# Kernel optimization log

Measured on AMD Instinct MI355X. Metric: run time of the kernel, lower is better.

The kernel has to match this reference:

```python
import jax, jax.numpy as jnp
import numpy as np

# SigKernel config (from init_kwargs)
SCALES = np.array([1.0], dtype=np.float32)
S0, S1 = 0.0, 1.0   # s0, S
T0, T1 = 0.0, 1.0   # t0, T
REFINEMENT = 1.0    # refinement_factor (new grid == old grid => interp is identity)


def _interpolate(X, t_min, t_max, refinement_factor):
    """Linear interpolation of batched paths (B, L, D) onto a refined uniform grid."""
    L = X.shape[1]
    new_L = int(refinement_factor * (L - 1)) + 1
    t = jnp.linspace(t_min, t_max, L)
    t_new = jnp.linspace(t_min, t_max, new_L)
    interp_ch = lambda ch: jnp.interp(t_new, t, ch)            # (L,) -> (new_L,)
    interp_path = lambda p: jax.vmap(interp_ch, in_axes=1, out_axes=1)(p)
    return jax.vmap(interp_path)(X)


def _solve_pde_single(inc):
    """Second-order finite-difference Goursat solve of K_st = inc * K.

    inc: (m, m) increment matrix. Returns K[m, m] (scalar), with boundary K[i,0]=K[0,j]=1.
    Wavefront recursion over the 2m-1 interior antidiagonals via lax.scan; each
    diagonal is stored as a length-(m+1) vector indexed by the row i (col j = d - i).
    """
    m = inc.shape[0]
    n = m + 1
    idx = jnp.arange(n)
    K0 = jnp.where(idx == 0, 1.0, 0.0)   # antidiagonal d=0
    K1 = jnp.where(idx <= 1, 1.0, 0.0)   # antidiagonal d=1

    def step(carry, d):
        Km2, Km1 = carry                 # diagonals d-2, d-1
        j = d - idx
        ir = jnp.clip(idx - 1, 0, m - 1)
        jc = jnp.clip(j - 1, 0, m - 1)
        a = inc[ir, jc]                  # inc[i-1, j-1] along the diagonal
        f1 = 1.0 + 0.5 * a + (a * a) * (1.0 / 12.0)
        f2 = 1.0 - (a * a) * (1.0 / 12.0)
        # K[i,j] = (K[i,j-1] + K[i-1,j]) * f1 - K[i-1,j-1] * f2
        Kij = (Km1 + jnp.roll(Km1, 1)) * f1 - jnp.roll(Km2, 1) * f2
        Kd = jnp.where((idx == 0) | (j == 0), 1.0, Kij)      # boundary = 1
        Kd = jnp.where((j >= 0) & (j <= m), Kd, 0.0)         # off-diagonal mask
        return (Km1, Kd), None

    (_, Klast), _ = jax.lax.scan(step, (K0, K1), jnp.arange(2, 2 * m + 1))
    return Klast[m]  # K at (m, m)


def _sig_kernel_matrix(X, Y, scale):
    # linear static kernel k(x,y) = scale^2 <x,y>  =>  grid increments of k
    dX = X[:, 1:, :] - X[:, :-1, :]   # (bx, m, d)
    dY = Y[:, 1:, :] - Y[:, :-1, :]   # (by, m, d)
    inc = (scale * scale) * jnp.einsum('aic,bjc->abij', dX, dY)  # (bx, by, m, m)
    return jax.vmap(jax.vmap(_solve_pde_single))(inc)            # (bx, by)


def reference(X, Y):
    Xi = _interpolate(X, S0, S1, REFINEMENT)
    Yi = _interpolate(Y, T0, T1, REFINEMENT)
    scales = jnp.asarray(SCALES)
    ks = jax.vmap(lambda s: _sig_kernel_matrix(Xi, Yi, s))(scales)
    return jnp.mean(ks, axis=0)


def setup_inputs() -> dict:
    key = jax.random.key(0)
    kx, ky = jax.random.split(key)
    bx, by, L, d = 32, 32, 256, 8
    # 0.05 scaling keeps the (exponentially growing) PDE solution well-conditioned
    X = 0.05 * jax.random.normal(kx, (bx, L, d), dtype=jnp.float32)
    Y = 0.05 * jax.random.normal(ky, (by, L, d), dtype=jnp.float32)
    return {"X": X, "Y": Y}
```

## Files before the change

### kernel.cpp

```cpp
#include <hip/hip_runtime.h>


typedef float f32x2 __attribute__((ext_vector_type(2)));
typedef float f32x4 __attribute__((ext_vector_type(4)));

#define MM     255
#define NINC   255
#define DYCOLS 324

static __device__ inline f32x2 fma2(f32x2 a, f32x2 b, f32x2 c) {
    return __builtin_elementwise_fma(a, b, c);
}

static __device__ inline float dpp_shr1(float old, float x) {
    int r = __builtin_amdgcn_update_dpp(
        __float_as_int(old), __float_as_int(x),
        0x138 , 0xF, 0xF, false);
    return __int_as_float(r);
}

static __device__ inline void pk_mul_bl(f32x2& d, f32x2 a, f32x2 b) {
    asm("v_pk_mul_f32 %0, %1, %2 op_sel:[0,0] op_sel_hi:[1,0]"
        : "=v"(d) : "v"(a), "v"(b));
}
static __device__ inline void pk_fma_bl(f32x2& d, f32x2 a, f32x2 b) {
    asm("v_pk_fma_f32 %0, %1, %2, %0 op_sel:[0,0,0] op_sel_hi:[1,0,1]"
        : "+v"(d) : "v"(a), "v"(b));
}
static __device__ inline void pk_fma_bh(f32x2& d, f32x2 a, f32x2 b) {
    asm("v_pk_fma_f32 %0, %1, %2, %0 op_sel:[0,1,0] op_sel_hi:[1,1,1]"
        : "+v"(d) : "v"(a), "v"(b));
}

__global__ __launch_bounds__(64) void sigker_opsel(
    const float* __restrict__ X,
    const float* __restrict__ Y,
    float* __restrict__ out)
{
    const int pair = blockIdx.x;
    const int ax = pair >> 5;
    const int by = pair & 31;
    const int l  = threadIdx.x;

    __shared__ f32x4 dYv[DYCOLS * 2];

    const float* Xa = X + ax * 2048;
    const float* Yb = Y + by * 2048;

    for (int v = l; v < (DYCOLS - NINC) * 2; v += 64)
        dYv[NINC * 2 + v] = (f32x4){0, 0, 0, 0};

    {
        f32x4 g[10];
        const f32x4* Yv = (const f32x4*)(Yb + l * 32);
        #pragma unroll
        for (int k = 0; k < 8; ++k) g[k] = Yv[k];
        g[8] = (l < 63) ? Yv[8] : (f32x4){0, 0, 0, 0};
        g[9] = (l < 63) ? Yv[9] : (f32x4){0, 0, 0, 0};
        #pragma unroll
        for (int r = 0; r < 4; ++r) {
            const int ji = 4 * l + r;
            if (ji < NINC) {
                f32x4 d0, d1;
                #pragma unroll
                for (int c = 0; c < 4; ++c) {
                    const int e = r * 8 + c;
                    d0[c] = g[(e + 8) >> 2][(e + 8) & 3] - g[e >> 2][e & 3];
                }
                #pragma unroll
                for (int c = 4; c < 8; ++c) {
                    const int e = r * 8 + c;
                    d1[c - 4] = g[(e + 8) >> 2][(e + 8) & 3] - g[e >> 2][e & 3];
                }
                dYv[2 * ji]     = d0;
                dYv[2 * ji + 1] = d1;
            }
        }
    }

    f32x2 dxp0[8], dxp1[8];
    {
        f32x4 f[10];
        const f32x4* Xv = (const f32x4*)(Xa + l * 32);
        #pragma unroll
        for (int k = 0; k < 8; ++k) f[k] = Xv[k];
        f[8] = (l < 63) ? Xv[8] : (f32x4){0, 0, 0, 0};
        f[9] = (l < 63) ? Xv[9] : (f32x4){0, 0, 0, 0};
        #pragma unroll
        for (int c = 0; c < 8; ++c) {
            const float e0 = f[(c)      >> 2][(c)      & 3];
            const float e1 = f[(8 + c)  >> 2][(8 + c)  & 3];
            const float e2 = f[(16 + c) >> 2][(16 + c) & 3];
            const float e3 = f[(24 + c) >> 2][(24 + c) & 3];
            const float e4 = f[(32 + c) >> 2][(32 + c) & 3];
            dxp0[c] = (f32x2){e1 - e0, e2 - e1};
            dxp1[c] = (f32x2){e3 - e2, e4 - e3};
        }
    }
    __syncthreads();

    const f32x2 C12  = { 1.0f / 12.0f,  1.0f / 12.0f};
    const f32x2 CN12 = {-1.0f / 12.0f, -1.0f / 12.0f};
    const f32x2 CH   = { 0.5f, 0.5f};
    const f32x2 C1   = { 1.0f, 1.0f};

    f32x2 dyp[4];
    f32x2 f1a, f1b, f2a, f2b;

    auto factors = [&]() {
        f32x2 a01, a23;
        pk_mul_bl(a01, dxp0[0], dyp[0]);  pk_mul_bl(a23, dxp1[0], dyp[0]);
        pk_fma_bh(a01, dxp0[1], dyp[0]);  pk_fma_bh(a23, dxp1[1], dyp[0]);
        pk_fma_bl(a01, dxp0[2], dyp[1]);  pk_fma_bl(a23, dxp1[2], dyp[1]);
        pk_fma_bh(a01, dxp0[3], dyp[1]);  pk_fma_bh(a23, dxp1[3], dyp[1]);
        pk_fma_bl(a01, dxp0[4], dyp[2]);  pk_fma_bl(a23, dxp1[4], dyp[2]);
        pk_fma_bh(a01, dxp0[5], dyp[2]);  pk_fma_bh(a23, dxp1[5], dyp[2]);
        pk_fma_bl(a01, dxp0[6], dyp[3]);  pk_fma_bl(a23, dxp1[6], dyp[3]);
        pk_fma_bh(a01, dxp0[7], dyp[3]);  pk_fma_bh(a23, dxp1[7], dyp[3]);
        const f32x2 q01 = a01 * a01, q23 = a23 * a23;
        f1a = fma2(q01, C12, fma2(a01, CH, C1));
        f1b = fma2(q23, C12, fma2(a23, CH, C1));
        f2a = fma2(q01, CN12, C1);
        f2b = fma2(q23, CN12, C1);
    };

    {
        const bool isL0 = (l == 0);
        const f32x4 i0 = dYv[0], i1 = dYv[1];
        dyp[0] = isL0 ? (f32x2){i0.x, i0.y} : (f32x2){0, 0};
        dyp[1] = isL0 ? (f32x2){i0.z, i0.w} : (f32x2){0, 0};
        dyp[2] = isL0 ? (f32x2){i1.x, i1.y} : (f32x2){0, 0};
        dyp[3] = isL0 ? (f32x2){i1.z, i1.w} : (f32x2){0, 0};
    }
    factors();

    f32x4 bcA = dYv[2], bcB = dYv[3];
    const f32x4* pf = &dYv[4];

    float K0 = 1.0f, K1 = 1.0f, K2 = 1.0f, K3 = 1.0f, upd = 1.0f;

    #pragma unroll 2
    for (int s = 1; s <= MM + 63; ++s) {
        const f32x4 nA = pf[0];
        const f32x4 nB = pf[1];
        pf += 2;

        const float up = dpp_shr1(1.0f, K3);
        const float t0 = upd * f2a.x;
        const float t1 = K0  * f2a.y;
        const float t2 = K1  * f2b.x;
        const float t3 = K2  * f2b.y;
        const float c0 = fmaf(K0, f1a.x, -t0);
        const float c1 = fmaf(K1, f1a.y, -t1);
        const float c2 = fmaf(K2, f1b.x, -t2);
        const float c3 = fmaf(K3, f1b.y, -t3);
        const float k0 = fmaf(up, f1a.x, c0);
        const float k1 = fmaf(k0, f1a.y, c1);
        const float k2 = fmaf(k1, f1b.x, c2);
        const float k3 = fmaf(k2, f1b.y, c3);
        upd = up; K0 = k0; K1 = k1; K2 = k2; K3 = k3;

        dyp[0].x = dpp_shr1(bcA.x, dyp[0].x);
        dyp[0].y = dpp_shr1(bcA.y, dyp[0].y);
        dyp[1].x = dpp_shr1(bcA.z, dyp[1].x);
        dyp[1].y = dpp_shr1(bcA.w, dyp[1].y);
        dyp[2].x = dpp_shr1(bcB.x, dyp[2].x);
        dyp[2].y = dpp_shr1(bcB.y, dyp[2].y);
        dyp[3].x = dpp_shr1(bcB.z, dyp[3].x);
        dyp[3].y = dpp_shr1(bcB.w, dyp[3].y);

        factors();

        bcA = nA; bcB = nB;
    }

    if (l == 63) out[pair] = K2;
}

extern "C" void kernel_launch(void* const* d_in, const int* in_sizes, int n_in,
                              void* d_out, int out_size, void* d_ws, size_t ws_size,
                              hipStream_t stream)
{
    const float* X = (const float*)d_in[0];
    const float* Y = (const float*)d_in[1];
    float* out = (float*)d_out;
    (void)in_sizes; (void)n_in; (void)out_size; (void)d_ws; (void)ws_size;

    sigker_opsel<<<dim3(32 * 32), dim3(64), 0, stream>>>(X, Y, out);
}
```

Measured before the change: 42.33 us.

## Process two Y paths per block with interleaved wavefront recurrences and skewed LDS columns

Each 64-thread block now solves two (x,y) pairs that share the same X path. The two independent recurrences are interleaved to hide each other's serial dependency latency. The dy increments are no longer shifted across lanes with DPP every step. Instead they are stored in LDS with a per-lane skew and zero padding, so each lane reads its own column directly. This halves the grid to 512 blocks and doubles register and LDS use per block. The __syncthreads was removed even though LDS is written and read across lanes, which relies on a single wave executing in lockstep.

```diff
diff --git a/kernel.cpp b/kernel.cpp
--- a/kernel.cpp
+++ b/kernel.cpp
@@ -4,9 +4,8 @@
 typedef float f32x2 __attribute__((ext_vector_type(2)));
 typedef float f32x4 __attribute__((ext_vector_type(4)));
 
-#define MM     255
-#define NINC   255
-#define DYCOLS 324
+#define NCOLS 384
+#define COLF  12
 
 static __device__ inline f32x2 fma2(f32x2 a, f32x2 b, f32x2 c) {
     return __builtin_elementwise_fma(a, b, c);
@@ -32,35 +31,46 @@
         : "+v"(d) : "v"(a), "v"(b));
 }
 
-__global__ __launch_bounds__(64) void sigker_opsel(
+__global__ __launch_bounds__(64) void sigker_twopair(
     const float* __restrict__ X,
     const float* __restrict__ Y,
     float* __restrict__ out)
 {
-    const int pair = blockIdx.x;
-    const int ax = pair >> 5;
-    const int by = pair & 31;
-    const int l  = threadIdx.x;
-
-    __shared__ f32x4 dYv[DYCOLS * 2];
-
-    const float* Xa = X + ax * 2048;
-    const float* Yb = Y + by * 2048;
-
-    for (int v = l; v < (DYCOLS - NINC) * 2; v += 64)
-        dYv[NINC * 2 + v] = (f32x4){0, 0, 0, 0};
-
-    {
+    const int b   = blockIdx.x;
+    const int ax  = b >> 4;
+    const int byA = (b & 15) << 1;
+    const int byB = byA + 1;
+    const int l   = threadIdx.x;
+
+    __shared__ float dYs[2][NCOLS * COLF];
+
+    const f32x4 zz = (f32x4){0, 0, 0, 0};
+
+    #pragma unroll
+    for (int p = 0; p < 2; ++p) {
+        f32x4* Z = (f32x4*)dYs[p];
+        if (l < 63) { Z[3*l] = zz; Z[3*l+1] = zz; Z[3*l+2] = zz; }
+        const int c = 318 + l;
+        Z[3*c] = zz; Z[3*c+1] = zz; Z[3*c+2] = zz;
+        if (l < 2) {
+            const int c2 = 382 + l;
+            Z[3*c2] = zz; Z[3*c2+1] = zz; Z[3*c2+2] = zz;
+        }
+    }
+
+    #pragma unroll
+    for (int p = 0; p < 2; ++p) {
+        const float* Yb = Y + (p ? byB : byA) * 2048;
         f32x4 g[10];
         const f32x4* Yv = (const f32x4*)(Yb + l * 32);
         #pragma unroll
         for (int k = 0; k < 8; ++k) g[k] = Yv[k];
-        g[8] = (l < 63) ? Yv[8] : (f32x4){0, 0, 0, 0};
-        g[9] = (l < 63) ? Yv[9] : (f32x4){0, 0, 0, 0};
+        g[8] = (l < 63) ? Yv[8] : zz;
+        g[9] = (l < 63) ? Yv[9] : zz;
         #pragma unroll
         for (int r = 0; r < 4; ++r) {
             const int ji = 4 * l + r;
-            if (ji < NINC) {
+            if (ji < 255) {
                 f32x4 d0, d1;
                 #pragma unroll
                 for (int c = 0; c < 4; ++c) {
@@ -72,20 +82,22 @@
                     const int e = r * 8 + c;
                     d1[c - 4] = g[(e + 8) >> 2][(e + 8) & 3] - g[e >> 2][e & 3];
                 }
-                dYv[2 * ji]     = d0;
-                dYv[2 * ji + 1] = d1;
+                f32x4* W = (f32x4*)(dYs[p] + (ji + 63) * COLF);
+                W[0] = d0;
+                W[1] = d1;
             }
         }
     }
 
     f32x2 dxp0[8], dxp1[8];
     {
+        const float* Xa = X + ax * 2048;
         f32x4 f[10];
         const f32x4* Xv = (const f32x4*)(Xa + l * 32);
         #pragma unroll
         for (int k = 0; k < 8; ++k) f[k] = Xv[k];
-        f[8] = (l < 63) ? Xv[8] : (f32x4){0, 0, 0, 0};
-        f[9] = (l < 63) ? Xv[9] : (f32x4){0, 0, 0, 0};
+        f[8] = (l < 63) ? Xv[8] : zz;
+        f[9] = (l < 63) ? Xv[9] : zz;
         #pragma unroll
         for (int c = 0; c < 8; ++c) {
             const float e0 = f[(c)      >> 2][(c)      & 3];
@@ -97,26 +109,32 @@
             dxp1[c] = (f32x2){e3 - e2, e4 - e3};
         }
     }
-    __syncthreads();
 
     const f32x2 C12  = { 1.0f / 12.0f,  1.0f / 12.0f};
     const f32x2 CN12 = {-1.0f / 12.0f, -1.0f / 12.0f};
     const f32x2 CH   = { 0.5f, 0.5f};
     const f32x2 C1   = { 1.0f, 1.0f};
 
-    f32x2 dyp[4];
-    f32x2 f1a, f1b, f2a, f2b;
-
-    auto factors = [&]() {
+    auto ldcol = [](const float* p, f32x2 d[4]) {
+        const f32x4* q = (const f32x4*)p;
+        const f32x4 t0 = q[0], t1 = q[1];
+        d[0] = __builtin_shufflevector(t0, t0, 0, 1);
+        d[1] = __builtin_shufflevector(t0, t0, 2, 3);
+        d[2] = __builtin_shufflevector(t1, t1, 0, 1);
+        d[3] = __builtin_shufflevector(t1, t1, 2, 3);
+    };
+
+    auto factors = [&](const f32x2 dy[4], f32x2& f1a, f32x2& f1b,
+                       f32x2& f2a, f32x2& f2b) {
         f32x2 a01, a23;
-        pk_mul_bl(a01, dxp0[0], dyp[0]);  pk_mul_bl(a23, dxp1[0], dyp[0]);
-        pk_fma_bh(a01, dxp0[1], dyp[0]);  pk_fma_bh(a23, dxp1[1], dyp[0]);
-        pk_fma_bl(a01, dxp0[2], dyp[1]);  pk_fma_bl(a23, dxp1[2], dyp[1]);
-        pk_fma_bh(a01, dxp0[3], dyp[1]);  pk_fma_bh(a23, dxp1[3], dyp[1]);
-        pk_fma_bl(a01, dxp0[4], dyp[2]);  pk_fma_bl(a23, dxp1[4], dyp[2]);
-        pk_fma_bh(a01, dxp0[5], dyp[2]);  pk_fma_bh(a23, dxp1[5], dyp[2]);
-        pk_fma_bl(a01, dxp0[6], dyp[3]);  pk_fma_bl(a23, dxp1[6], dyp[3]);
-        pk_fma_bh(a01, dxp0[7], dyp[3]);  pk_fma_bh(a23, dxp1[7], dyp[3]);
+        pk_mul_bl(a01, dxp0[0], dy[0]);  pk_mul_bl(a23, dxp1[0], dy[0]);
+        pk_fma_bh(a01, dxp0[1], dy[0]);  pk_fma_bh(a23, dxp1[1], dy[0]);
+        pk_fma_bl(a01, dxp0[2], dy[1]);  pk_fma_bl(a23, dxp1[2], dy[1]);
+        pk_fma_bh(a01, dxp0[3], dy[1]);  pk_fma_bh(a23, dxp1[3], dy[1]);
+        pk_fma_bl(a01, dxp0[4], dy[2]);  pk_fma_bl(a23, dxp1[4], dy[2]);
+        pk_fma_bh(a01, dxp0[5], dy[2]);  pk_fma_bh(a23, dxp1[5], dy[2]);
+        pk_fma_bl(a01, dxp0[6], dy[3]);  pk_fma_bl(a23, dxp1[6], dy[3]);
+        pk_fma_bh(a01, dxp0[7], dy[3]);  pk_fma_bh(a23, dxp1[7], dy[3]);
         const f32x2 q01 = a01 * a01, q23 = a23 * a23;
         f1a = fma2(q01, C12, fma2(a01, CH, C1));
         f1b = fma2(q23, C12, fma2(a23, CH, C1));
@@ -124,57 +142,72 @@
         f2b = fma2(q23, CN12, C1);
     };
 
+    float KA0 = 1.0f, KA1 = 1.0f, KA2 = 1.0f, KA3 = 1.0f, updA = 1.0f;
+    float KB0 = 1.0f, KB1 = 1.0f, KB2 = 1.0f, KB3 = 1.0f, updB = 1.0f;
+    f32x2 f1aA, f1bA, f2aA, f2bA;
+    f32x2 f1aB, f1bB, f2aB, f2bB;
+
+    const float* pa = dYs[0] + (63 - l) * COLF;
+    const float* pb = dYs[1] + (63 - l) * COLF;
     {
-        const bool isL0 = (l == 0);
-        const f32x4 i0 = dYv[0], i1 = dYv[1];
-        dyp[0] = isL0 ? (f32x2){i0.x, i0.y} : (f32x2){0, 0};
-        dyp[1] = isL0 ? (f32x2){i0.z, i0.w} : (f32x2){0, 0};
-        dyp[2] = isL0 ? (f32x2){i1.x, i1.y} : (f32x2){0, 0};
-        dyp[3] = isL0 ? (f32x2){i1.z, i1.w} : (f32x2){0, 0};
-    }
-    factors();
-
-    f32x4 bcA = dYv[2], bcB = dYv[3];
-    const f32x4* pf = &dYv[4];
-
-    float K0 = 1.0f, K1 = 1.0f, K2 = 1.0f, K3 = 1.0f, upd = 1.0f;
+        f32x2 dyA[4], dyB[4];
+        ldcol(pa, dyA);
+        ldcol(pb, dyB);
+        factors(dyA, f1aA, f1bA, f2aA, f2bA);
+        factors(dyB, f1aB, f1bB, f2aB, f2bB);
+    }
+    pa += COLF;
+    pb += COLF;
 
     #pragma unroll 2
-    for (int s = 1; s <= MM + 63; ++s) {
-        const f32x4 nA = pf[0];
-        const f32x4 nB = pf[1];
-        pf += 2;
-
-        const float up = dpp_shr1(1.0f, K3);
-        const float t0 = upd * f2a.x;
-        const float t1 = K0  * f2a.y;
-        const float t2 = K1  * f2b.x;
-        const float t3 = K2  * f2b.y;
-        const float c0 = fmaf(K0, f1a.x, -t0);
-        const float c1 = fmaf(K1, f1a.y, -t1);
-        const float c2 = fmaf(K2, f1b.x, -t2);
-        const float c3 = fmaf(K3, f1b.y, -t3);
-        const float k0 = fmaf(up, f1a.x, c0);
-        const float k1 = fmaf(k0, f1a.y, c1);
-        const float k2 = fmaf(k1, f1b.x, c2);
-        const float k3 = fmaf(k2, f1b.y, c3);
-        upd = up; K0 = k0; K1 = k1; K2 = k2; K3 = k3;
-
-        dyp[0].x = dpp_shr1(bcA.x, dyp[0].x);
-        dyp[0].y = dpp_shr1(bcA.y, dyp[0].y);
-        dyp[1].x = dpp_shr1(bcA.z, dyp[1].x);
-        dyp[1].y = dpp_shr1(bcA.w, dyp[1].y);
-        dyp[2].x = dpp_shr1(bcB.x, dyp[2].x);
-        dyp[2].y = dpp_shr1(bcB.y, dyp[2].y);
-        dyp[3].x = dpp_shr1(bcB.z, dyp[3].x);
-        dyp[3].y = dpp_shr1(bcB.w, dyp[3].y);
-
-        factors();
-
-        bcA = nA; bcB = nB;
-    }
-
-    if (l == 63) out[pair] = K2;
+    for (int s = 1; s <= 318; ++s) {
+        f32x2 nA[4], nB[4];
+        ldcol(pa, nA);
+        ldcol(pb, nB);
+        pa += COLF;
+        pb += COLF;
+
+        {
+            const float up = dpp_shr1(1.0f, KA3);
+            const float t0 = updA * f2aA.x;
+            const float t1 = KA0  * f2aA.y;
+            const float t2 = KA1  * f2bA.x;
+            const float t3 = KA2  * f2bA.y;
+            const float c0 = fmaf(KA0, f1aA.x, -t0);
+            const float c1 = fmaf(KA1, f1aA.y, -t1);
+            const float c2 = fmaf(KA2, f1bA.x, -t2);
+            const float c3 = fmaf(KA3, f1bA.y, -t3);
+            const float k0 = fmaf(up, f1aA.x, c0);
+            const float k1 = fmaf(k0, f1aA.y, c1);
+            const float k2 = fmaf(k1, f1bA.x, c2);
+            const float k3 = fmaf(k2, f1bA.y, c3);
+            updA = up; KA0 = k0; KA1 = k1; KA2 = k2; KA3 = k3;
+        }
+        {
+            const float up = dpp_shr1(1.0f, KB3);
+            const float t0 = updB * f2aB.x;
+            const float t1 = KB0  * f2aB.y;
+            const float t2 = KB1  * f2bB.x;
+            const float t3 = KB2  * f2bB.y;
+            const float c0 = fmaf(KB0, f1aB.x, -t0);
+            const float c1 = fmaf(KB1, f1aB.y, -t1);
+            const float c2 = fmaf(KB2, f1bB.x, -t2);
+            const float c3 = fmaf(KB3, f1bB.y, -t3);
+            const float k0 = fmaf(up, f1aB.x, c0);
+            const float k1 = fmaf(k0, f1aB.y, c1);
+            const float k2 = fmaf(k1, f1bB.x, c2);
+            const float k3 = fmaf(k2, f1bB.y, c3);
+            updB = up; KB0 = k0; KB1 = k1; KB2 = k2; KB3 = k3;
+        }
+
+        factors(nA, f1aA, f1bA, f2aA, f2bA);
+        factors(nB, f1aB, f1bB, f2aB, f2bB);
+    }
+
+    if (l == 63) {
+        out[2 * b]     = KA2;
+        out[2 * b + 1] = KB2;
+    }
 }
 
 extern "C" void kernel_launch(void* const* d_in, const int* in_sizes, int n_in,
@@ -186,5 +219,5 @@
     float* out = (float*)d_out;
     (void)in_sizes; (void)n_in; (void)out_size; (void)d_ws; (void)ws_size;
 
-    sigker_opsel<<<dim3(32 * 32), dim3(64), 0, stream>>>(X, Y, out);
-}
+    sigker_twopair<<<dim3(512), dim3(64), 0, stream>>>(X, Y, out);
+}
```

Result: slower. 61.80 us (+46.0%).
